# Kernel optimization log

Measured on AMD Instinct MI355X. Metric: run time of the kernel, lower is better.

The kernel has to match this reference:

```python
import jax, jax.numpy as jnp
import numpy as np

N = 8192        # nodes
E = 131072      # template edges (avg degree 16)
IN_DIM = 2
H = 128         # hidden_dim
Z = 128         # z_dim
MAX_DEPTH = 32
DEPTH_PERTURB = 2
NEG = -1e30


def setup_inputs() -> dict:
    key = jax.random.key(0)
    ks = jax.random.split(key, 24)
    s = 0.05
    # template node features: col0 = node type in {0,1,2}, col1 = placeholder
    types = jax.random.randint(ks[0], (N,), 0, 3)
    x = jnp.stack([types.astype(jnp.float32),
                   jax.random.normal(ks[1], (N,))], axis=1)
    edge_index = jax.random.randint(ks[2], (2, E), 0, N)
    node_depth = jnp.sort(jax.random.randint(ks[3], (N,), 0, MAX_DEPTH))
    z = jax.random.normal(ks[4], (Z,))
    return {
        "x": x, "z": z,
        "edge_index": edge_index, "node_depth": node_depth,
        # GCNConv 1 & 2 (PyG style: y = x @ W^T, symmetric-normalized agg, + bias)
        "conv1_w": jax.random.normal(ks[5], (H, IN_DIM)) * s,
        "conv1_b": jnp.zeros((H,)),
        "conv2_w": jax.random.normal(ks[6], (H, H)) * s,
        "conv2_b": jnp.zeros((H,)),
        # node_proj: Linear(H+Z,H) -> ReLU -> Linear(H,H)
        "np1_w": jax.random.normal(ks[7], (H, H + Z)) * s,
        "np1_b": jnp.zeros((H,)),
        "np2_w": jax.random.normal(ks[8], (H, H)) * s,
        "np2_b": jnp.zeros((H,)),
        # src/tgt projections (bias-free)
        "src_w": jax.random.normal(ks[9], (H, H)) * s,
        "tgt_w": jax.random.normal(ks[10], (H, H)) * s,
        # inv_mlp: Linear(2H+Z,H) -> ReLU -> Linear(H,1)
        "inv1_w": jax.random.normal(ks[11], (H, 2 * H + Z)) * s,
        "inv1_b": jnp.zeros((H,)),
        "inv2_w": jax.random.normal(ks[12], (1, H)) * s,
        "inv2_b": jnp.zeros((1,)),
    }


def _gcn_conv(x, src, dst, W, b, n):
    # PyG GCNConv with self loops: out_i = sum_j norm_ij * (x_j W^T) + b
    xw = x @ W.T                                             # [n, out]
    deg = jax.ops.segment_sum(jnp.ones(src.shape, xw.dtype), dst,
                              num_segments=n) + 1.0          # self-loop
    rsq = jax.lax.rsqrt(deg)
    msg = (rsq[src] * rsq[dst])[:, None] * xw[src]           # [E, out]
    agg = jax.ops.segment_sum(msg, dst, num_segments=n)
    agg = agg + xw / deg[:, None]                            # self-loop term
    return agg + b


def reference(x, z, edge_index, node_depth,
              conv1_w, conv1_b, conv2_w, conv2_b,
              np1_w, np1_b, np2_w, np2_b,
              src_w, tgt_w, inv1_w, inv1_b, inv2_w, inv2_b):
    n = x.shape[0]
    types = x[:, 0].astype(jnp.int32)
    src, dst = edge_index[0], edge_index[1]

    # --- GCN encode ---
    h = jax.nn.relu(_gcn_conv(x, src, dst, conv1_w, conv1_b, n))
    h = jax.nn.relu(_gcn_conv(h, src, dst, conv2_w, conv2_b, n))

    # --- node_proj with broadcast z ---
    hz = jnp.concatenate([h, jnp.broadcast_to(z[None, :], (n, Z))], axis=1)
    h = jax.nn.relu(hz @ np1_w.T + np1_b) @ np2_w.T + np2_b  # [n, H]

    # --- vectorized per-target candidate attention scores ---
    Ht = h @ tgt_w.T                                         # [n, H]
    Hs = h @ src_w.T                                         # [n, H]
    scores = Ht @ Hs.T                                       # [n, n]: S[v,u]
    depth = node_depth
    # candidate u valid for target v iff depth[u] <= depth[v]-1+perturb
    cand_mask = depth[None, :] <= (depth[:, None] - 1 + DEPTH_PERTURB)
    scores_m = jnp.where(cand_mask, scores, NEG)
    top_vals, top_idx = jax.lax.top_k(scores_m, 2)           # [n,2] each

    num_cand = cand_mask.sum(axis=1)
    target_valid = (depth >= 1) & (types != 0)
    # type==2 (AND) gets k=2 fanins, other non-PI types k=1
    valid = jnp.stack([target_valid & (num_cand >= 1),
                       target_valid & (types == 2) & (num_cand >= 2)], axis=1)

    # --- per-edge inversion-bit MLP (vectorized over [n, 2] chosen edges) ---
    h_u = h[top_idx]                                         # [n,2,H]
    h_v = jnp.broadcast_to(h[:, None, :], (n, 2, H))
    z_b = jnp.broadcast_to(z[None, None, :], (n, 2, Z))
    inv_in = jnp.concatenate([h_u, h_v, z_b], axis=-1)       # [n,2,2H+Z]
    inv_logit = (jax.nn.relu(inv_in @ inv1_w.T + inv1_b) @ inv2_w.T + inv2_b)[..., 0]
    inv_bit = (jax.nn.sigmoid(inv_logit) > 0.5).astype(jnp.int32)

    return top_vals, inv_logit, top_idx, inv_bit, valid
```

## Files before the change

kernel.cpp:

```cpp
#include <hip/hip_runtime.h>

#define NN 8192
#define EE 131072
#define HH 128
#define NEGV -1.0e30f
#define SEG 128
#define NSEG (NN / SEG)
#define VT 128

typedef __attribute__((ext_vector_type(8))) short bf16x8;
typedef __attribute__((ext_vector_type(4))) float f32x4;

typedef __attribute__((address_space(1))) unsigned int AS1U;
typedef __attribute__((address_space(3))) unsigned int AS3U;

__device__ __forceinline__ unsigned short f2bf(float f) {
    unsigned int u = __float_as_uint(f);
    unsigned int r = u + 0x7fffu + ((u >> 16) & 1u);
    return (unsigned short)(r >> 16);
}
__device__ __forceinline__ float bf2f(unsigned short b) {
    return __uint_as_float((unsigned int)b << 16);
}


__global__ __launch_bounds__(256) void k_init(const int* __restrict__ edst, int* __restrict__ degi,
                                              const float* __restrict__ conv2_w, const float* __restrict__ np1_w,
                                              const float* __restrict__ np2_w, const float* __restrict__ src_w,
                                              const float* __restrict__ tgt_w, const float* __restrict__ inv1_w,
                                              const float* __restrict__ np1_b, const float* __restrict__ inv1_b,
                                              const float* __restrict__ z, float* __restrict__ T,
                                              float* __restrict__ c1, float* __restrict__ cz,
                                              const int* __restrict__ depth, const float* __restrict__ x,
                                              int* __restrict__ cnt, float* __restrict__ out,
                                              int* __restrict__ cursor, int* __restrict__ tctr) {
    int b = blockIdx.x;
    int tid = threadIdx.x;
    if (b < 512) {
        int t = b * 256 + tid;
        atomicAdd(&degi[edst[t]], 1);
    } else if (b < 1024) {
        int tb = b - 512;
        int y = tb >> 6, xb = tb & 63;
        if (y < 7) {
            int t = xb * 256 + tid;
            int j = t >> 7, k = t & 127;
            const float* W; int stride, off;
            switch (y) {
                case 0:  W = conv2_w; stride = 128; off = 0;   break;
                case 1:  W = np1_w;   stride = 256; off = 0;   break;
                case 2:  W = np2_w;   stride = 128; off = 0;   break;
                case 3:  W = src_w;   stride = 128; off = 0;   break;
                case 4:  W = tgt_w;   stride = 128; off = 0;   break;
                case 5:  W = inv1_w;  stride = 384; off = 0;   break;
                default: W = inv1_w;  stride = 384; off = 128; break;
            }
            T[y * 16384 + k * 128 + j] = W[j * stride + off + k];
        } else if (xb == 0) {
            if (tid < 128) {
                float s = np1_b[tid];
                for (int k = 0; k < 128; k++) s += z[k] * np1_w[tid * 256 + 128 + k];
                c1[tid] = s;
            } else {
                int j = tid - 128;
                float s = inv1_b[j];
                for (int k = 0; k < 128; k++) s += z[k] * inv1_w[j * 384 + 256 + k];
                cz[j] = s;
            }
        }
    } else if (b < 1056) {
        int v = (b - 1024) * 256 + tid;
        int limit = depth[v] + 1;
        int lo = 0, hi = NN;
        while (lo < hi) { int mid = (lo + hi) >> 1; if (depth[mid] <= limit) lo = mid + 1; else hi = mid; }
        cnt[v] = lo;
        int type = (int)(x[v * 2] + 0.5f);
        bool tv = (depth[v] >= 1) && (type != 0);
        out[4 * NN * 2 + v * 2 + 0] = (tv && lo >= 1) ? 1.0f : 0.0f;
        out[4 * NN * 2 + v * 2 + 1] = (tv && type == 2 && lo >= 2) ? 1.0f : 0.0f;
    } else {
#pragma unroll
        for (int i = 0; i < 32; i++) cursor[i * 256 + tid] = 0;
        if (tid == 0) *tctr = 0;
    }
}


__global__ __launch_bounds__(1024) void k_scan_tiles(const int* __restrict__ degi, int* __restrict__ rowptr,
                                                     float* __restrict__ dinv, float* __restrict__ rsq,
                                                     const int* __restrict__ cnt, int* __restrict__ nact,
                                                     int* __restrict__ tlist, int* __restrict__ ntiles) {
    if (blockIdx.x == 0) {
        __shared__ int ls[1024];
        int tid = threadIdx.x;
        int base = tid * 8;
        int loc[8]; int s = 0;
#pragma unroll
        for (int i = 0; i < 8; i++) {
            int dg = degi[base + i];
            loc[i] = s; s += dg;
            double d = (double)(dg + 1);
            dinv[base + i] = (float)(1.0 / d);
            rsq[base + i] = (float)(1.0 / sqrt(d));
        }
        ls[tid] = s; __syncthreads();
        int tot = s;
        for (int d = 1; d < 1024; d <<= 1) {
            int v = (tid >= d) ? ls[tid - d] : 0;
            __syncthreads();
            ls[tid] += v;
            __syncthreads();
        }
        int pre = ls[tid] - tot;
#pragma unroll
        for (int i = 0; i < 8; i++) rowptr[base + i] = pre + loc[i];
        if (tid == 1023) rowptr[NN] = pre + tot;
    } else {
        int lane = threadIdx.x;
        if (lane >= 64) return;
        int cmax = cnt[lane * VT + VT - 1];
        int n = (cmax + SEG - 1) / SEG;
        nact[lane] = n;
        int x = n;
        for (int off = 1; off < 64; off <<= 1) {
            int y = __shfl_up(x, off, 64);
            if (lane >= off) x += y;
        }
        int base = x - n;
        for (int s = 0; s < n; s++) tlist[base + s] = (lane << 8) | s;
        if (lane == 63) *ntiles = x;
    }
}

__global__ __launch_bounds__(256) void k_fill(const int* __restrict__ src, const int* __restrict__ dst,
                                              const int* __restrict__ rowptr, int* __restrict__ cursor,
                                              int* __restrict__ ecsr) {
    int t = blockIdx.x * 256 + threadIdx.x;
    if (t < EE) {
        int d = dst[t];
        int pos = atomicAdd(&cursor[d], 1);
        ecsr[rowptr[d] + pos] = src[t];
    }
}


__global__ __launch_bounds__(256) void k_gather1xw(const int* __restrict__ rowptr, const int* __restrict__ ecsr,
                                                   const float* __restrict__ rsq, const float* __restrict__ dinv,
                                                   const float* __restrict__ x, const float* __restrict__ w,
                                                   const float* __restrict__ bias, const float* __restrict__ T0,
                                                   float* __restrict__ xw2) {
    __shared__ float h1s[4][128];
    int tid = threadIdx.x;
    int g = blockIdx.x * 256 + tid;
    int d = g >> 6, lane = g & 63, wv = tid >> 6;
    {
        float w0a = w[lane * 2], w1a = w[lane * 2 + 1];
        float w0b = w[(lane + 64) * 2], w1b = w[(lane + 64) * 2 + 1];
        int s0 = rowptr[d], s1 = rowptr[d + 1];
        float rd = rsq[d];
        float a0 = 0.f, a1 = 0.f;
        for (int sl = s0; sl < s1; sl++) {
            int s = ecsr[sl];
            float x0 = x[s * 2], x1 = x[s * 2 + 1];
            float f = rsq[s] * rd;
            a0 = fmaf(f, x0 * w0a + x1 * w1a, a0);
            a1 = fmaf(f, x0 * w0b + x1 * w1b, a1);
        }
        float x0d = x[d * 2], x1d = x[d * 2 + 1], di = dinv[d];
        a0 = fmaf(x0d * w0a + x1d * w1a, di, a0) + bias[lane];
        a1 = fmaf(x0d * w0b + x1d * w1b, di, a1) + bias[64 + lane];
        h1s[wv][lane] = fmaxf(a0, 0.f);
        h1s[wv][64 + lane] = fmaxf(a1, 0.f);
    }
    __syncthreads();
    int j = tid & 127, r0 = tid >> 7;
    int dbase = blockIdx.x * 4;
    float acc0 = 0.f, acc1 = 0.f;
#pragma unroll 8
    for (int k = 0; k < 128; k++) {
        float t0 = T0[k * 128 + j];
        acc0 = fmaf(h1s[r0][k], t0, acc0);
        acc1 = fmaf(h1s[r0 + 2][k], t0, acc1);
    }
    xw2[(size_t)(dbase + r0) * HH + j] = acc0;
    xw2[(size_t)(dbase + r0 + 2) * HH + j] = acc1;
}


__global__ __launch_bounds__(256) void k_gather2(const int* __restrict__ rowptr, const int* __restrict__ ecsr,
                                                 const float* __restrict__ rsq, const float* __restrict__ dinv,
                                                 const float* __restrict__ xw, const float* __restrict__ bias,
                                                 float* __restrict__ out) {
    int g = blockIdx.x * 256 + threadIdx.x;
    int d = g >> 6, lane = g & 63;
    if (d >= NN) return;
    int s0 = rowptr[d], s1 = rowptr[d + 1];
    float rd = rsq[d];
    float a0 = 0.f, a1 = 0.f;
    for (int sl = s0; sl < s1; sl++) {
        int s = ecsr[sl];
        float f = rsq[s] * rd;
        a0 = fmaf(f, xw[s * HH + lane], a0);
        a1 = fmaf(f, xw[s * HH + 64 + lane], a1);
    }
    float di = dinv[d];
    a0 = fmaf(xw[d * HH + lane], di, a0) + bias[lane];
    a1 = fmaf(xw[d * HH + 64 + lane], di, a1) + bias[64 + lane];
    out[d * HH + lane] = fmaxf(a0, 0.f);
    out[d * HH + 64 + lane] = fmaxf(a1, 0.f);
}


__global__ __launch_bounds__(256) void k_mlp(const float* __restrict__ h2g, const float* __restrict__ T,
                                             const float* __restrict__ c1, const float* __restrict__ np2_b,
                                             float* __restrict__ h3g,
                                             unsigned short* __restrict__ HtP, unsigned short* __restrict__ HsP) {
    __shared__ float bufA[32][132];
    __shared__ float bufB[32][132];
    __shared__ float Bs[32][128];
    int tid = threadIdx.x;
    int tx = tid & 31, ty = tid >> 5;
    int row0 = blockIdx.x * 32;
#pragma unroll
    for (int p = 0; p < 4; p++) {
        int q = p * 256 + tid;
        int r = q >> 5, c4 = (q & 31) * 4;
        *(float4*)&bufA[r][c4] = *(const float4*)&h2g[(size_t)(row0 + r) * HH + c4];
    }
    __syncthreads();
    for (int g = 0; g < 4; g++) {
        const float* WT;
        switch (g) {
            case 0:  WT = T + 1 * 16384; break;
            case 1:  WT = T + 2 * 16384; break;
            case 2:  WT = T + 4 * 16384; break;
            default: WT = T + 3 * 16384; break;
        }
        float (*src)[132] = (g == 1) ? bufB : bufA;
        float acc[4][4] = {};
        for (int k0 = 0; k0 < 128; k0 += 32) {
#pragma unroll
            for (int i = 0; i < 4; i++) {
                int kk = (tid >> 5) + i * 8;
                int c = (tid & 31) << 2;
                *(float4*)&Bs[kk][c] = *(const float4*)&WT[(k0 + kk) * HH + c];
            }
            __syncthreads();
#pragma unroll 8
            for (int kk = 0; kk < 32; kk++) {
                float a0 = src[ty * 4 + 0][k0 + kk], a1 = src[ty * 4 + 1][k0 + kk];
                float a2 = src[ty * 4 + 2][k0 + kk], a3 = src[ty * 4 + 3][k0 + kk];
                float4 b = *(const float4*)&Bs[kk][tx * 4];
                acc[0][0] = fmaf(a0, b.x, acc[0][0]); acc[0][1] = fmaf(a0, b.y, acc[0][1]);
                acc[0][2] = fmaf(a0, b.z, acc[0][2]); acc[0][3] = fmaf(a0, b.w, acc[0][3]);
                acc[1][0] = fmaf(a1, b.x, acc[1][0]); acc[1][1] = fmaf(a1, b.y, acc[1][1]);
                acc[1][2] = fmaf(a1, b.z, acc[1][2]); acc[1][3] = fmaf(a1, b.w, acc[1][3]);
                acc[2][0] = fmaf(a2, b.x, acc[2][0]); acc[2][1] = fmaf(a2, b.y, acc[2][1]);
                acc[2][2] = fmaf(a2, b.z, acc[2][2]); acc[2][3] = fmaf(a2, b.w, acc[2][3]);
                acc[3][0] = fmaf(a3, b.x, acc[3][0]); acc[3][1] = fmaf(a3, b.y, acc[3][1]);
                acc[3][2] = fmaf(a3, b.z, acc[3][2]); acc[3][3] = fmaf(a3, b.w, acc[3][3]);
            }
            __syncthreads();
        }
        if (g == 0) {
#pragma unroll
            for (int i = 0; i < 4; i++)
#pragma unroll
                for (int jj = 0; jj < 4; jj++)
                    bufB[ty * 4 + i][tx * 4 + jj] = fmaxf(acc[i][jj] + c1[tx * 4 + jj], 0.f);
        } else if (g == 1) {
#pragma unroll
            for (int i = 0; i < 4; i++) {
                float4 v;
                v.x = acc[i][0] + np2_b[tx * 4 + 0];
                v.y = acc[i][1] + np2_b[tx * 4 + 1];
                v.z = acc[i][2] + np2_b[tx * 4 + 2];
                v.w = acc[i][3] + np2_b[tx * 4 + 3];
                bufA[ty * 4 + i][tx * 4 + 0] = v.x; bufA[ty * 4 + i][tx * 4 + 1] = v.y;
                bufA[ty * 4 + i][tx * 4 + 2] = v.z; bufA[ty * 4 + i][tx * 4 + 3] = v.w;
                *(float4*)&h3g[(size_t)(row0 + ty * 4 + i) * HH + tx * 4] = v;
            }
        } else {
            unsigned short* PP = (g == 2) ? HtP : HsP;
            int chunk = tx >> 3;
            int cic = (tx * 4) & 31;
#pragma unroll
            for (int i = 0; i < 4; i++) {
                int row = row0 + ty * 4 + i;
                size_t off = (size_t)row * 384 + chunk * 96 + cic;
                unsigned short h[4], m[4], lo[4];
#pragma unroll
                for (int jj = 0; jj < 4; jj++) {
                    float val = acc[i][jj];
                    unsigned short hb = f2bf(val);
                    float r1 = val - bf2f(hb);
                    unsigned short mb = f2bf(r1);
                    float r2 = r1 - bf2f(mb);
                    h[jj] = hb; m[jj] = mb; lo[jj] = f2bf(r2);
                }
                *(uint2*)&PP[off] = make_uint2((unsigned)h[0] | ((unsigned)h[1] << 16),
                                               (unsigned)h[2] | ((unsigned)h[3] << 16));
                *(uint2*)&PP[off + 32] = make_uint2((unsigned)m[0] | ((unsigned)m[1] << 16),
                                                    (unsigned)m[2] | ((unsigned)m[3] << 16));
                *(uint2*)&PP[off + 64] = make_uint2((unsigned)lo[0] | ((unsigned)lo[1] << 16),
                                                    (unsigned)lo[2] | ((unsigned)lo[3] << 16));
            }
        }
    }
}


__device__ __forceinline__ void stage32(unsigned short* buf, const unsigned short* __restrict__ HsP,
                                        int cb, int wave, int lane) {
    if (lane < 48) {
        const unsigned short* g0 = HsP + (size_t)(cb + wave * 4) * 384 + lane * 8;
        unsigned short* l0 = buf + wave * 4 * 392;
#pragma unroll
        for (int k = 0; k < 4; k++) {
            __builtin_amdgcn_global_load_lds((const AS1U*)(g0 + (size_t)k * 384),
                                             (AS3U*)(l0 + k * 392), 16, 0, 0);
        }
    }
}

__global__ __launch_bounds__(512, 4) void k_top2_stage1(
    const unsigned short* __restrict__ HtP, const unsigned short* __restrict__ HsP,
    const int* __restrict__ cnt, const int* __restrict__ tlist,
    const int* __restrict__ ntiles, int* __restrict__ tctr,
    float* __restrict__ pval, int* __restrict__ pidx) {
    __shared__ unsigned short Bsh[2][32 * 392];
    __shared__ int tsh;
    int tid = threadIdx.x;
    int wave = tid >> 6, lane = tid & 63;
    int l = lane & 15, quad = lane >> 4;
    int nt = *ntiles;
    for (;;) {
        __syncthreads();
        if (tid == 0) tsh = atomicAdd(tctr, 1);
        __syncthreads();
        int t = tsh;
        if (t >= nt) return;
        int code = tlist[t];
        int v0 = (code >> 8) * VT;
        int seg = code & 255;
        int ub0 = seg * SEG;
        int vbase = v0 + wave * 16;
        int cmax = cnt[v0 + VT - 1];
        int uend = ub0 + SEG; if (uend > cmax) uend = cmax;
        int nch = (uend - ub0 + 31) >> 5;
        stage32(Bsh[0], HsP, ub0, wave, lane);
        bf16x8 afr[4][3];
        {
            const unsigned short* ap = &HtP[(size_t)(vbase + l) * 384 + quad * 8];
#pragma unroll
            for (int c = 0; c < 4; c++) {
                afr[c][0] = *(const bf16x8*)&ap[c * 96];
                afr[c][1] = *(const bf16x8*)&ap[c * 96 + 32];
                afr[c][2] = *(const bf16x8*)&ap[c * 96 + 64];
            }
        }
        int creg[4];
#pragma unroll
        for (int i = 0; i < 4; i++)
            creg[i] = cnt[vbase + quad * 4 + i];
        float t1v[4], t2v[4]; int t1i[4], t2i[4];
#pragma unroll
        for (int i = 0; i < 4; i++) { t1v[i] = NEGV; t2v[i] = NEGV; t1i[i] = 0x7fffffff; t2i[i] = 0x7fffffff; }
        __syncthreads();
        for (int ci = 0; ci < nch; ci++) {
            int cb = ub0 + ci * 32;
            if (ci + 1 < nch) stage32(Bsh[(ci + 1) & 1], HsP, cb + 32, wave, lane);
            const unsigned short* bbase = Bsh[ci & 1];
            int cend = cb + 32; if (cend > uend) cend = uend;
            for (int u0 = cb; u0 < cend; u0 += 16) {
                int u = u0 + l;
                const unsigned short* bp = &bbase[(u0 - cb + l) * 392 + quad * 8];
                f32x4 acc0 = {0.f, 0.f, 0.f, 0.f};
#pragma unroll
                for (int c = 0; c < 4; c++) {
                    bf16x8 bh = *(const bf16x8*)&bp[c * 96];
                    bf16x8 bm = *(const bf16x8*)&bp[c * 96 + 32];
                    bf16x8 bl = *(const bf16x8*)&bp[c * 96 + 64];
                    acc0 = __builtin_amdgcn_mfma_f32_16x16x32_bf16(afr[c][0], bh, acc0, 0, 0, 0);
                    acc0 = __builtin_amdgcn_mfma_f32_16x16x32_bf16(afr[c][0], bm, acc0, 0, 0, 0);
                    acc0 = __builtin_amdgcn_mfma_f32_16x16x32_bf16(afr[c][1], bh, acc0, 0, 0, 0);
                    acc0 = __builtin_amdgcn_mfma_f32_16x16x32_bf16(afr[c][0], bl, acc0, 0, 0, 0);
                    acc0 = __builtin_amdgcn_mfma_f32_16x16x32_bf16(afr[c][2], bh, acc0, 0, 0, 0);
                    acc0 = __builtin_amdgcn_mfma_f32_16x16x32_bf16(afr[c][1], bm, acc0, 0, 0, 0);
                }
#pragma unroll
                for (int i = 0; i < 4; i++) {
                    float sv = acc0[i];
                    bool gt1 = (u < creg[i]) & (sv > t1v[i]);
                    bool gt2 = (u < creg[i]) & (sv > t2v[i]);
                    float n2v = gt1 ? t1v[i] : (gt2 ? sv : t2v[i]);
                    int   n2i = gt1 ? t1i[i] : (gt2 ? u  : t2i[i]);
                    t1v[i] = gt1 ? sv : t1v[i];
                    t1i[i] = gt1 ? u  : t1i[i];
                    t2v[i] = n2v; t2i[i] = n2i;
                }
            }
            __syncthreads();
        }
#pragma unroll
        for (int m = 1; m <= 8; m <<= 1) {
#pragma unroll
            for (int i = 0; i < 4; i++) {
                float ov1 = __shfl_xor(t1v[i], m, 64);
                int   oi1 = __shfl_xor(t1i[i], m, 64);
                float ov2 = __shfl_xor(t2v[i], m, 64);
                int   oi2 = __shfl_xor(t2i[i], m, 64);
                bool b1 = (ov1 > t1v[i]) || (ov1 == t1v[i] && oi1 < t1i[i]);
                float w1v = b1 ? ov1 : t1v[i]; int w1i = b1 ? oi1 : t1i[i];
                float l1v = b1 ? t1v[i] : ov1; int l1i = b1 ? t1i[i] : oi1;
                float c2v = b1 ? ov2 : t2v[i]; int c2i = b1 ? oi2 : t2i[i];
                bool b2 = (l1v > c2v) || (l1v == c2v && l1i < c2i);
                t1v[i] = w1v; t1i[i] = w1i;
                t2v[i] = b2 ? l1v : c2v; t2i[i] = b2 ? l1i : c2i;
            }
        }
        if (l == 0) {
#pragma unroll
            for (int i = 0; i < 4; i++) {
                int v = vbase + quad * 4 + i;
                int o = (v * NSEG + seg) * 2;
                pval[o] = t1v[i];     pidx[o] = t1i[i];
                pval[o + 1] = t2v[i]; pidx[o + 1] = t2i[i];
            }
        }
    }
}


__global__ __launch_bounds__(256) void k_merge_inv(const float* __restrict__ pval, const int* __restrict__ pidx,
                                                   const int* __restrict__ nact,
                                                   const float* __restrict__ h3, const float* __restrict__ T5,
                                                   const float* __restrict__ T6,
                                                   const float* __restrict__ cz, const float* __restrict__ w2,
                                                   const float* __restrict__ b2, float* __restrict__ out) {
    __shared__ float rows[4][3][128];
    int gid = blockIdx.x * 256 + threadIdx.x;
    int v = gid >> 6, lane = gid & 63;
    int wv = threadIdx.x >> 6;
    if (v >= NN) return;
    int na = nact[v >> 7];
    float v1 = NEGV, v2 = NEGV; int i1 = 0x7fffffff, i2 = 0x7fffffff;
    if (lane < na) {
        int o = (v * NSEG + lane) * 2;
        v1 = pval[o];     i1 = pidx[o];
        v2 = pval[o + 1]; i2 = pidx[o + 1];
    }
#pragma unroll
    for (int m = 1; m <= 32; m <<= 1) {
        float ov1 = __shfl_xor(v1, m, 64);
        int   oi1 = __shfl_xor(i1, m, 64);
        float ov2 = __shfl_xor(v2, m, 64);
        int   oi2 = __shfl_xor(i2, m, 64);
        bool b1 = (ov1 > v1) || (ov1 == v1 && oi1 < i1);
        float w1v = b1 ? ov1 : v1; int w1i = b1 ? oi1 : i1;
        float l1v = b1 ? v1 : ov1; int l1i = b1 ? i1 : oi1;
        float c2v = b1 ? ov2 : v2; int c2i = b1 ? oi2 : i2;
        bool b2 = (l1v > c2v) || (l1v == c2v && l1i < c2i);
        v1 = w1v; i1 = w1i;
        v2 = b2 ? l1v : c2v; i2 = b2 ? l1i : c2i;
    }
    if (v1 == NEGV) { v2 = NEGV; i1 = 0; i2 = 1; }
    else if (v2 == NEGV) { i2 = (i1 == 0) ? 1 : 0; }
    int u1 = i1, u2 = i2;
    rows[wv][0][lane] = h3[(size_t)u1 * HH + lane]; rows[wv][0][64 + lane] = h3[(size_t)u1 * HH + 64 + lane];
    rows[wv][1][lane] = h3[(size_t)u2 * HH + lane]; rows[wv][1][64 + lane] = h3[(size_t)u2 * HH + 64 + lane];
    rows[wv][2][lane] = h3[(size_t)v * HH + lane];  rows[wv][2][64 + lane] = h3[(size_t)v * HH + 64 + lane];
    float pa0 = 0.f, pa1 = 0.f, pb0 = 0.f, pb1 = 0.f, qa = 0.f, qb = 0.f;
#pragma unroll 8
    for (int k = 0; k < 128; k++) {
        float hu1 = rows[wv][0][k];
        float hu2 = rows[wv][1][k];
        float hv  = rows[wv][2][k];
        float t5a = T5[k * 128 + lane], t5b = T5[k * 128 + 64 + lane];
        float t6a = T6[k * 128 + lane], t6b = T6[k * 128 + 64 + lane];
        pa0 = fmaf(hu1, t5a, pa0); pa1 = fmaf(hu1, t5b, pa1);
        pb0 = fmaf(hu2, t5a, pb0); pb1 = fmaf(hu2, t5b, pb1);
        qa  = fmaf(hv,  t6a, qa);  qb  = fmaf(hv,  t6b, qb);
    }
    float cza = cz[lane], czb = cz[64 + lane];
    float w2a = w2[lane], w2b = w2[64 + lane];
    float p0 = fmaxf(pa0 + qa + cza, 0.f) * w2a + fmaxf(pa1 + qb + czb, 0.f) * w2b;
    float p1 = fmaxf(pb0 + qa + cza, 0.f) * w2a + fmaxf(pb1 + qb + czb, 0.f) * w2b;
#pragma unroll
    for (int off = 32; off >= 1; off >>= 1) {
        p0 += __shfl_down(p0, off, 64);
        p1 += __shfl_down(p1, off, 64);
    }
    if (lane == 0) {
        float bb = b2[0];
        float l0 = p0 + bb, l1 = p1 + bb;
        out[v * 2 + 0] = v1; out[v * 2 + 1] = v2;
        out[NN * 2 + v * 2 + 0] = l0;
        out[NN * 2 + v * 2 + 1] = l1;
        out[2 * NN * 2 + v * 2 + 0] = (float)i1;
        out[2 * NN * 2 + v * 2 + 1] = (float)i2;
        out[3 * NN * 2 + v * 2 + 0] = (l0 > 0.f) ? 1.f : 0.f;
        out[3 * NN * 2 + v * 2 + 1] = (l1 > 0.f) ? 1.f : 0.f;
    }
}


extern "C" void kernel_launch(void* const* d_in, const int* in_sizes, int n_in,
                              void* d_out, int out_size, void* d_ws, size_t ws_size,
                              hipStream_t stream) {
    const float* x       = (const float*)d_in[0];
    const float* z       = (const float*)d_in[1];
    const int*   eidx    = (const int*)d_in[2];
    const int*   depth   = (const int*)d_in[3];
    const float* conv1_w = (const float*)d_in[4];
    const float* conv1_b = (const float*)d_in[5];
    const float* conv2_w = (const float*)d_in[6];
    const float* conv2_b = (const float*)d_in[7];
    const float* np1_w   = (const float*)d_in[8];
    const float* np1_b   = (const float*)d_in[9];
    const float* np2_w   = (const float*)d_in[10];
    const float* np2_b   = (const float*)d_in[11];
    const float* src_w   = (const float*)d_in[12];
    const float* tgt_w   = (const float*)d_in[13];
    const float* inv1_w  = (const float*)d_in[14];
    const float* inv1_b  = (const float*)d_in[15];
    const float* inv2_w  = (const float*)d_in[16];
    const float* inv2_b  = (const float*)d_in[17];
    float* out = (float*)d_out;
    float* wsf = (float*)d_ws;

    const int NH = NN * HH;
    float* R0 = wsf;
    float* R1 = wsf + (size_t)NH;
    unsigned short* HtP = (unsigned short*)R1;
    unsigned short* HsP = HtP + 3 * (size_t)NH;
    float* pval = wsf + 4 * (size_t)NH;
    int*   pidx = (int*)(wsf + 5 * (size_t)NH);
    float* T  = wsf + 6 * (size_t)NH;
    float* c1 = T + 7 * 16384;
    float* cz = c1 + 128;
    float* rsq  = cz + 128;
    float* dinv = rsq + NN;
    int* degi   = (int*)(dinv + NN);
    int* rowptr = degi + NN;
    int* cursor = rowptr + NN + 1;
    int* cnt    = cursor + NN;
    int* nact   = cnt + NN;
    int* ntiles = nact + 64;
    int* tctr   = ntiles + 1;
    int* tlist  = tctr + 1;
    int* ecsr   = tlist + 4096;

    const int* esrc = eidx;
    const int* edst = eidx + EE;

    hipMemsetAsync(degi, 0, NN * sizeof(int), stream);
    k_init<<<1057, 256, 0, stream>>>(edst, degi, conv2_w, np1_w, np2_w, src_w, tgt_w, inv1_w,
                                     np1_b, inv1_b, z, T, c1, cz, depth, x, cnt, out, cursor, tctr);
    k_scan_tiles<<<2, 1024, 0, stream>>>(degi, rowptr, dinv, rsq, cnt, nact, tlist, ntiles);
    k_fill<<<EE / 256, 256, 0, stream>>>(esrc, edst, rowptr, cursor, ecsr);
    k_gather1xw<<<NN * 64 / 256, 256, 0, stream>>>(rowptr, ecsr, rsq, dinv, x, conv1_w, conv1_b,
                                                   T + 0 * 16384, R1);
    k_gather2<<<NN * 64 / 256, 256, 0, stream>>>(rowptr, ecsr, rsq, dinv, R1, conv2_b, R0);
    k_mlp<<<256, 256, 0, stream>>>(R0, T, c1, np2_b, R0, HtP, HsP);
    k_top2_stage1<<<768, 512, 0, stream>>>(HtP, HsP, cnt, tlist, ntiles, tctr, pval, pidx);
    k_merge_inv<<<NN / 4, 256, 0, stream>>>(pval, pidx, nact, R0, T + 5 * 16384, T + 6 * 16384,
                                            cz, inv2_w, inv2_b, out);
}
```

Measured before the change: 298.4 us.

## Precompute per-node inversion-MLP projections via GEMM and halve MLP tile rows

The per-vertex inversion MLP used to redo the first-layer matvec for each (u, v) pair inside k_merge_inv. It now precomputes P = h3·W5 and Q = h3·W6 for all nodes in a dense GEMM kernel, so the merge kernel only gathers rows and applies ReLU and the dot product. Separately, k_mlp row tiles are cut from 32 to 16 with twice as many blocks, to improve occupancy. The trade-off is an extra kernel launch, extra global traffic for P and Q (which reuse the now-dead HtP/HsP workspace), and less register reuse per thread in the GEMMs.

```diff
diff --git a/kernel.cpp b/kernel.cpp
--- a/kernel.cpp
+++ b/kernel.cpp
@@ -215,14 +215,14 @@
                                              const float* __restrict__ c1, const float* __restrict__ np2_b,
                                              float* __restrict__ h3g,
                                              unsigned short* __restrict__ HtP, unsigned short* __restrict__ HsP) {
-    __shared__ float bufA[32][132];
-    __shared__ float bufB[32][132];
+    __shared__ float bufA[16][132];
+    __shared__ float bufB[16][132];
     __shared__ float Bs[32][128];
     int tid = threadIdx.x;
     int tx = tid & 31, ty = tid >> 5;
-    int row0 = blockIdx.x * 32;
-#pragma unroll
-    for (int p = 0; p < 4; p++) {
+    int row0 = blockIdx.x * 16;
+#pragma unroll
+    for (int p = 0; p < 2; p++) {
         int q = p * 256 + tid;
         int r = q >> 5, c4 = (q & 31) * 4;
         *(float4*)&bufA[r][c4] = *(const float4*)&h2g[(size_t)(row0 + r) * HH + c4];
@@ -237,7 +237,7 @@
             default: WT = T + 3 * 16384; break;
         }
         float (*src)[132] = (g == 1) ? bufB : bufA;
-        float acc[4][4] = {};
+        float acc[2][4] = {};
         for (int k0 = 0; k0 < 128; k0 += 32) {
 #pragma unroll
             for (int i = 0; i < 4; i++) {
@@ -248,45 +248,40 @@
             __syncthreads();
 #pragma unroll 8
             for (int kk = 0; kk < 32; kk++) {
-                float a0 = src[ty * 4 + 0][k0 + kk], a1 = src[ty * 4 + 1][k0 + kk];
-                float a2 = src[ty * 4 + 2][k0 + kk], a3 = src[ty * 4 + 3][k0 + kk];
+                float a0 = src[ty * 2 + 0][k0 + kk], a1 = src[ty * 2 + 1][k0 + kk];
                 float4 b = *(const float4*)&Bs[kk][tx * 4];
                 acc[0][0] = fmaf(a0, b.x, acc[0][0]); acc[0][1] = fmaf(a0, b.y, acc[0][1]);
                 acc[0][2] = fmaf(a0, b.z, acc[0][2]); acc[0][3] = fmaf(a0, b.w, acc[0][3]);
                 acc[1][0] = fmaf(a1, b.x, acc[1][0]); acc[1][1] = fmaf(a1, b.y, acc[1][1]);
                 acc[1][2] = fmaf(a1, b.z, acc[1][2]); acc[1][3] = fmaf(a1, b.w, acc[1][3]);
-                acc[2][0] = fmaf(a2, b.x, acc[2][0]); acc[2][1] = fmaf(a2, b.y, acc[2][1]);
-                acc[2][2] = fmaf(a2, b.z, acc[2][2]); acc[2][3] = fmaf(a2, b.w, acc[2][3]);
-                acc[3][0] = fmaf(a3, b.x, acc[3][0]); acc[3][1] = fmaf(a3, b.y, acc[3][1]);
-                acc[3][2] = fmaf(a3, b.z, acc[3][2]); acc[3][3] = fmaf(a3, b.w, acc[3][3]);
             }
             __syncthreads();
         }
         if (g == 0) {
 #pragma unroll
-            for (int i = 0; i < 4; i++)
+            for (int i = 0; i < 2; i++)
 #pragma unroll
                 for (int jj = 0; jj < 4; jj++)
-                    bufB[ty * 4 + i][tx * 4 + jj] = fmaxf(acc[i][jj] + c1[tx * 4 + jj], 0.f);
+                    bufB[ty * 2 + i][tx * 4 + jj] = fmaxf(acc[i][jj] + c1[tx * 4 + jj], 0.f);
         } else if (g == 1) {
 #pragma unroll
-            for (int i = 0; i < 4; i++) {
+            for (int i = 0; i < 2; i++) {
                 float4 v;
                 v.x = acc[i][0] + np2_b[tx * 4 + 0];
                 v.y = acc[i][1] + np2_b[tx * 4 + 1];
                 v.z = acc[i][2] + np2_b[tx * 4 + 2];
                 v.w = acc[i][3] + np2_b[tx * 4 + 3];
-                bufA[ty * 4 + i][tx * 4 + 0] = v.x; bufA[ty * 4 + i][tx * 4 + 1] = v.y;
-                bufA[ty * 4 + i][tx * 4 + 2] = v.z; bufA[ty * 4 + i][tx * 4 + 3] = v.w;
-                *(float4*)&h3g[(size_t)(row0 + ty * 4 + i) * HH + tx * 4] = v;
+                bufA[ty * 2 + i][tx * 4 + 0] = v.x; bufA[ty * 2 + i][tx * 4 + 1] = v.y;
+                bufA[ty * 2 + i][tx * 4 + 2] = v.z; bufA[ty * 2 + i][tx * 4 + 3] = v.w;
+                *(float4*)&h3g[(size_t)(row0 + ty * 2 + i) * HH + tx * 4] = v;
             }
         } else {
             unsigned short* PP = (g == 2) ? HtP : HsP;
             int chunk = tx >> 3;
             int cic = (tx * 4) & 31;
 #pragma unroll
-            for (int i = 0; i < 4; i++) {
-                int row = row0 + ty * 4 + i;
+            for (int i = 0; i < 2; i++) {
+                int row = row0 + ty * 2 + i;
                 size_t off = (size_t)row * 384 + chunk * 96 + cic;
                 unsigned short h[4], m[4], lo[4];
 #pragma unroll
@@ -305,6 +300,53 @@
                 *(uint2*)&PP[off + 64] = make_uint2((unsigned)lo[0] | ((unsigned)lo[1] << 16),
                                                     (unsigned)lo[2] | ((unsigned)lo[3] << 16));
             }
+        }
+    }
+}
+
+
+__global__ __launch_bounds__(256) void k_gemmPQ(const float* __restrict__ A, const float* __restrict__ WT0,
+                                                const float* __restrict__ WT1,
+                                                float* __restrict__ P, float* __restrict__ Q) {
+    __shared__ float As[16][132];
+    __shared__ float Bs[32][128];
+    int tid = threadIdx.x;
+    int tx = tid & 31, ty = tid >> 5;
+    int row0 = blockIdx.x * 16;
+#pragma unroll
+    for (int p = 0; p < 2; p++) {
+        int q = p * 256 + tid;
+        int r = q >> 5, c4 = (q & 31) * 4;
+        *(float4*)&As[r][c4] = *(const float4*)&A[(size_t)(row0 + r) * HH + c4];
+    }
+    __syncthreads();
+    for (int m = 0; m < 2; m++) {
+        const float* WT = m ? WT1 : WT0;
+        float* outp = m ? Q : P;
+        float acc[2][4] = {};
+        for (int k0 = 0; k0 < 128; k0 += 32) {
+#pragma unroll
+            for (int i = 0; i < 4; i++) {
+                int kk = (tid >> 5) + i * 8;
+                int c = (tid & 31) << 2;
+                *(float4*)&Bs[kk][c] = *(const float4*)&WT[(k0 + kk) * HH + c];
+            }
+            __syncthreads();
+#pragma unroll 8
+            for (int kk = 0; kk < 32; kk++) {
+                float a0 = As[ty * 2 + 0][k0 + kk], a1 = As[ty * 2 + 1][k0 + kk];
+                float4 b = *(const float4*)&Bs[kk][tx * 4];
+                acc[0][0] = fmaf(a0, b.x, acc[0][0]); acc[0][1] = fmaf(a0, b.y, acc[0][1]);
+                acc[0][2] = fmaf(a0, b.z, acc[0][2]); acc[0][3] = fmaf(a0, b.w, acc[0][3]);
+                acc[1][0] = fmaf(a1, b.x, acc[1][0]); acc[1][1] = fmaf(a1, b.y, acc[1][1]);
+                acc[1][2] = fmaf(a1, b.z, acc[1][2]); acc[1][3] = fmaf(a1, b.w, acc[1][3]);
+            }
+            __syncthreads();
+        }
+#pragma unroll
+        for (int i = 0; i < 2; i++) {
+            *(float4*)&outp[(size_t)(row0 + ty * 2 + i) * HH + tx * 4] =
+                make_float4(acc[i][0], acc[i][1], acc[i][2], acc[i][3]);
         }
     }
 }
@@ -434,14 +476,11 @@
 
 __global__ __launch_bounds__(256) void k_merge_inv(const float* __restrict__ pval, const int* __restrict__ pidx,
                                                    const int* __restrict__ nact,
-                                                   const float* __restrict__ h3, const float* __restrict__ T5,
-                                                   const float* __restrict__ T6,
+                                                   const float* __restrict__ P, const float* __restrict__ Q,
                                                    const float* __restrict__ cz, const float* __restrict__ w2,
                                                    const float* __restrict__ b2, float* __restrict__ out) {
-    __shared__ float rows[4][3][128];
     int gid = blockIdx.x * 256 + threadIdx.x;
     int v = gid >> 6, lane = gid & 63;
-    int wv = threadIdx.x >> 6;
     if (v >= NN) return;
     int na = nact[v >> 7];
     float v1 = NEGV, v2 = NEGV; int i1 = 0x7fffffff, i2 = 0x7fffffff;
@@ -467,25 +506,13 @@
     if (v1 == NEGV) { v2 = NEGV; i1 = 0; i2 = 1; }
     else if (v2 == NEGV) { i2 = (i1 == 0) ? 1 : 0; }
     int u1 = i1, u2 = i2;
-    rows[wv][0][lane] = h3[(size_t)u1 * HH + lane]; rows[wv][0][64 + lane] = h3[(size_t)u1 * HH + 64 + lane];
-    rows[wv][1][lane] = h3[(size_t)u2 * HH + lane]; rows[wv][1][64 + lane] = h3[(size_t)u2 * HH + 64 + lane];
-    rows[wv][2][lane] = h3[(size_t)v * HH + lane];  rows[wv][2][64 + lane] = h3[(size_t)v * HH + 64 + lane];
-    float pa0 = 0.f, pa1 = 0.f, pb0 = 0.f, pb1 = 0.f, qa = 0.f, qb = 0.f;
-#pragma unroll 8
-    for (int k = 0; k < 128; k++) {
-        float hu1 = rows[wv][0][k];
-        float hu2 = rows[wv][1][k];
-        float hv  = rows[wv][2][k];
-        float t5a = T5[k * 128 + lane], t5b = T5[k * 128 + 64 + lane];
-        float t6a = T6[k * 128 + lane], t6b = T6[k * 128 + 64 + lane];
-        pa0 = fmaf(hu1, t5a, pa0); pa1 = fmaf(hu1, t5b, pa1);
-        pb0 = fmaf(hu2, t5a, pb0); pb1 = fmaf(hu2, t5b, pb1);
-        qa  = fmaf(hv,  t6a, qa);  qb  = fmaf(hv,  t6b, qb);
-    }
     float cza = cz[lane], czb = cz[64 + lane];
     float w2a = w2[lane], w2b = w2[64 + lane];
-    float p0 = fmaxf(pa0 + qa + cza, 0.f) * w2a + fmaxf(pa1 + qb + czb, 0.f) * w2b;
-    float p1 = fmaxf(pb0 + qa + cza, 0.f) * w2a + fmaxf(pb1 + qb + czb, 0.f) * w2b;
+    float Qa = Q[(size_t)v * HH + lane], Qb = Q[(size_t)v * HH + 64 + lane];
+    float p0 = fmaxf(P[(size_t)u1 * HH + lane] + Qa + cza, 0.f) * w2a +
+               fmaxf(P[(size_t)u1 * HH + 64 + lane] + Qb + czb, 0.f) * w2b;
+    float p1 = fmaxf(P[(size_t)u2 * HH + lane] + Qa + cza, 0.f) * w2a +
+               fmaxf(P[(size_t)u2 * HH + 64 + lane] + Qb + czb, 0.f) * w2b;
 #pragma unroll
     for (int off = 32; off >= 1; off >>= 1) {
         p0 += __shfl_down(p0, off, 64);
@@ -534,6 +561,8 @@
     float* R1 = wsf + (size_t)NH;
     unsigned short* HtP = (unsigned short*)R1;
     unsigned short* HsP = HtP + 3 * (size_t)NH;
+    float* P = wsf + (size_t)NH;
+    float* Q = wsf + 2 * (size_t)NH;
     float* pval = wsf + 4 * (size_t)NH;
     int*   pidx = (int*)(wsf + 5 * (size_t)NH);
     float* T  = wsf + 6 * (size_t)NH;
@@ -562,8 +591,8 @@
     k_gather1xw<<<NN * 64 / 256, 256, 0, stream>>>(rowptr, ecsr, rsq, dinv, x, conv1_w, conv1_b,
                                                    T + 0 * 16384, R1);
     k_gather2<<<NN * 64 / 256, 256, 0, stream>>>(rowptr, ecsr, rsq, dinv, R1, conv2_b, R0);
-    k_mlp<<<256, 256, 0, stream>>>(R0, T, c1, np2_b, R0, HtP, HsP);
+    k_mlp<<<512, 256, 0, stream>>>(R0, T, c1, np2_b, R0, HtP, HsP);
     k_top2_stage1<<<768, 512, 0, stream>>>(HtP, HsP, cnt, tlist, ntiles, tctr, pval, pidx);
-    k_merge_inv<<<NN / 4, 256, 0, stream>>>(pval, pidx, nact, R0, T + 5 * 16384, T + 6 * 16384,
-                                            cz, inv2_w, inv2_b, out);
-}
+    k_gemmPQ<<<512, 256, 0, stream>>>(R0, T + 5 * 16384, T + 6 * 16384, P, Q);
+    k_merge_inv<<<NN / 4, 256, 0, stream>>>(pval, pidx, nact, P, Q, cz, inv2_w, inv2_b, out);
+}
```

Result: faster. 286.0 us (-4.1%).
